# Kernel optimization log

Hardware: AMD Instinct MI355X
Metric: run time of the kernel (lower is better)

The kernel has to match this reference:

```python
import jax, jax.numpy as jnp
import numpy as np

N = 100000
D = 512


def setup_inputs() -> dict:
    key = jax.random.key(0)
    k1, k2 = jax.random.split(key)
    features = jax.random.normal(k1, (N, D), dtype=jnp.float32)
    attn_w = jax.random.normal(k2, (D,), dtype=jnp.float32)
    attn_b = jnp.zeros((1,), dtype=jnp.float32)
    return {"features": features, "attn_w": attn_w, "attn_b": attn_b, "k": 4}


def reference(features, attn_w, attn_b, k):
    # features: [N, D]; sliding-window (half-width k, truncated at edges) mean
    n = features.shape[0]
    zero = jnp.zeros((1, features.shape[1]), dtype=features.dtype)
    cs = jnp.concatenate([zero, jnp.cumsum(features, axis=0)], axis=0)  # [N+1, D]
    i = jnp.arange(n)
    lo = jnp.maximum(i - k, 0)          # inclusive window start
    hi = jnp.minimum(i + k, n - 1)      # inclusive window end
    win_sum = cs[hi + 1] - cs[lo]       # [N, D]
    count = (hi - lo + 1).astype(features.dtype)[:, None]
    agg = win_sum / count               # [N, D] windowed means
    scores = agg @ attn_w + attn_b[0]   # [N]
    w = jax.nn.softmax(scores, axis=0)  # [N]
    bag = w @ agg                       # [D]
    return bag, w
```

## Files before the change

kernel.cpp:

```cpp
#include <hip/hip_runtime.h>
#include <math.h>

#define D 512
#define NB_P 1000

__global__ void k_dot(const float* __restrict__ f, const float* __restrict__ w,
                      float* __restrict__ dot, int n) {
    int wave = threadIdx.x >> 6;
    int lane = threadIdx.x & 63;
    int row  = blockIdx.x * 4 + wave;
    if (row >= n) return;
    const float4* fr = (const float4*)(f + (size_t)row * D);
    const float4* wr = (const float4*)w;
    float4 a0 = fr[lane],      b0 = wr[lane];
    float4 a1 = fr[lane + 64], b1 = wr[lane + 64];
    float s = a0.x*b0.x + a0.y*b0.y + a0.z*b0.z + a0.w*b0.w
            + a1.x*b1.x + a1.y*b1.y + a1.z*b1.z + a1.w*b1.w;
    #pragma unroll
    for (int off = 32; off; off >>= 1) s += __shfl_down(s, off);
    if (lane == 0) dot[row] = s;
}

__global__ void k_scores(const float* __restrict__ dot, const float* __restrict__ bptr,
                         const int* __restrict__ kptr, float* __restrict__ scores,
                         float* __restrict__ pmax, int n) {
    int i = blockIdx.x * blockDim.x + threadIdx.x;
    int k = *kptr;
    float val = -INFINITY;
    if (i < n) {
        int lo = max(i - k, 0), hi = min(i + k, n - 1);
        float s = 0.f;
        for (int j = lo; j <= hi; ++j) s += dot[j];
        val = s / (float)(hi - lo + 1) + bptr[0];
        scores[i] = val;
    }
    float m = val;
    #pragma unroll
    for (int off = 32; off; off >>= 1) m = fmaxf(m, __shfl_down(m, off));
    __shared__ float sm[4];
    int lane = threadIdx.x & 63, wid = threadIdx.x >> 6;
    if (lane == 0) sm[wid] = m;
    __syncthreads();
    if (threadIdx.x == 0) {
        float mm = fmaxf(fmaxf(sm[0], sm[1]), fmaxf(sm[2], sm[3]));
        pmax[blockIdx.x] = mm;
    }
}

__global__ void k_gmax(const float* __restrict__ pmax, int nb, float* __restrict__ scal) {
    float m = -INFINITY;
    for (int i = threadIdx.x; i < nb; i += blockDim.x) m = fmaxf(m, pmax[i]);
    #pragma unroll
    for (int off = 32; off; off >>= 1) m = fmaxf(m, __shfl_down(m, off));
    __shared__ float sm[4];
    int lane = threadIdx.x & 63, wid = threadIdx.x >> 6;
    if (lane == 0) sm[wid] = m;
    __syncthreads();
    if (threadIdx.x == 0) scal[0] = fmaxf(fmaxf(sm[0], sm[1]), fmaxf(sm[2], sm[3]));
}

__global__ void k_exp(float* __restrict__ scores, const float* __restrict__ scal,
                      float* __restrict__ psum, int n) {
    int i = blockIdx.x * blockDim.x + threadIdx.x;
    float gmax = scal[0];
    float e = 0.f;
    if (i < n) {
        e = expf(scores[i] - gmax);
        scores[i] = e;
    }
    #pragma unroll
    for (int off = 32; off; off >>= 1) e += __shfl_down(e, off);
    __shared__ float sm[4];
    int lane = threadIdx.x & 63, wid = threadIdx.x >> 6;
    if (lane == 0) sm[wid] = e;
    __syncthreads();
    if (threadIdx.x == 0) psum[blockIdx.x] = sm[0] + sm[1] + sm[2] + sm[3];
}

__global__ void k_gsum(const float* __restrict__ psum, int nb, float* __restrict__ scal) {
    float s = 0.f;
    for (int i = threadIdx.x; i < nb; i += blockDim.x) s += psum[i];
    #pragma unroll
    for (int off = 32; off; off >>= 1) s += __shfl_down(s, off);
    __shared__ float sm[4];
    int lane = threadIdx.x & 63, wid = threadIdx.x >> 6;
    if (lane == 0) sm[wid] = s;
    __syncthreads();
    if (threadIdx.x == 0) scal[1] = 1.f / (sm[0] + sm[1] + sm[2] + sm[3]);
}

__global__ void k_wu(const float* __restrict__ e, const float* __restrict__ scal,
                     const int* __restrict__ kptr, float* __restrict__ w_out,
                     float* __restrict__ u, int n) {
    int j = blockIdx.x * blockDim.x + threadIdx.x;
    if (j >= n) return;
    int k = *kptr;
    float inv = scal[1];
    w_out[j] = e[j] * inv;
    int lo = max(j - k, 0), hi = min(j + k, n - 1);
    float s = 0.f;
    for (int i = lo; i <= hi; ++i) {
        int li = max(i - k, 0), hh = min(i + k, n - 1);
        s += e[i] / (float)(hh - li + 1);
    }
    u[j] = s * inv;
}

__global__ void k_pbag(const float* __restrict__ f, const float* __restrict__ u,
                       float* __restrict__ partial, int n, int chunk) {
    int t = threadIdx.x;
    int j0 = blockIdx.x * chunk;
    int j1 = min(j0 + chunk, n);
    float4 acc = make_float4(0.f, 0.f, 0.f, 0.f);
    for (int j = j0; j < j1; ++j) {
        float uj = u[j];
        float4 v = ((const float4*)(f + (size_t)j * D))[t];
        acc.x += uj * v.x; acc.y += uj * v.y;
        acc.z += uj * v.z; acc.w += uj * v.w;
    }
    ((float4*)(partial + (size_t)blockIdx.x * D))[t] = acc;
}

__global__ void k_rbag(const float* __restrict__ partial, float* __restrict__ bag, int nb) {
    int c = blockIdx.x * 16 + (threadIdx.x & 15);
    int r = threadIdx.x >> 4;
    float acc = 0.f;
    for (int b = r; b < nb; b += 16) acc += partial[(size_t)b * D + c];
    __shared__ float sm[256];
    sm[threadIdx.x] = acc;
    __syncthreads();
    if (threadIdx.x < 16) {
        float s = 0.f;
        #pragma unroll
        for (int q = 0; q < 16; ++q) s += sm[q * 16 + threadIdx.x];
        bag[blockIdx.x * 16 + threadIdx.x] = s;
    }
}

extern "C" void kernel_launch(void* const* d_in, const int* in_sizes, int n_in,
                              void* d_out, int out_size, void* d_ws, size_t ws_size,
                              hipStream_t stream) {
    const float* f  = (const float*)d_in[0];
    const float* aw = (const float*)d_in[1];
    const float* ab = (const float*)d_in[2];
    const int*   kp = (const int*)d_in[3];
    int n = in_sizes[0] / D;

    float* bag   = (float*)d_out;
    float* w_out = (float*)d_out + D;

    float* wsf    = (float*)d_ws;
    int nb2       = (n + 255) / 256;
    float* dot    = wsf;
    float* scores = wsf + n;
    float* u      = wsf + 2 * (size_t)n;
    float* pmax   = wsf + 3 * (size_t)n;
    float* psum   = pmax + nb2;
    float* scal   = psum + nb2;
    size_t poff   = ((3 * (size_t)n + 2 * (size_t)nb2 + 2) + 15) & ~(size_t)15;
    float* partial = wsf + poff;

    int chunk = (n + NB_P - 1) / NB_P;

    k_dot   <<<(n + 3) / 4, 256, 0, stream>>>(f, aw, dot, n);
    k_scores<<<nb2, 256, 0, stream>>>(dot, ab, kp, scores, pmax, n);
    k_gmax  <<<1, 256, 0, stream>>>(pmax, nb2, scal);
    k_exp   <<<nb2, 256, 0, stream>>>(scores, scal, psum, n);
    k_gsum  <<<1, 256, 0, stream>>>(psum, nb2, scal);
    k_wu    <<<nb2, 256, 0, stream>>>(scores, scal, kp, w_out, u, n);
    k_pbag  <<<NB_P, 128, 0, stream>>>(f, u, partial, n, chunk);
    k_rbag  <<<32, 256, 0, stream>>>(partial, bag, NB_P);
}
```

Baseline: 99.66 us.

## Fuse softmax stages with online max-sum combine and unroll dot/bag kernels

Replaces the separate global-max, exp and sum kernels with an online-softmax scheme. Each score block now records its local max and rescaled exp sum, and one combine kernel merges them. Exponentials are recomputed inside k_wu instead of being stored, which cuts two launches and a pass over the scores. k_dot now handles two rows per wave, k_pbag unrolls by four with independent accumulators, and the number of bag partial blocks doubles. The costs are extra exp work in k_wu, fast-math exp and reciprocal, and a partial buffer twice as large to reduce.

```diff
diff --git a/kernel.cpp b/kernel.cpp
--- a/kernel.cpp
+++ b/kernel.cpp
@@ -2,29 +2,40 @@
 #include <math.h>
 
 #define D 512
-#define NB_P 1000
+#define NB_P 2000
 
 __global__ void k_dot(const float* __restrict__ f, const float* __restrict__ w,
                       float* __restrict__ dot, int n) {
-    int wave = threadIdx.x >> 6;
     int lane = threadIdx.x & 63;
-    int row  = blockIdx.x * 4 + wave;
-    if (row >= n) return;
-    const float4* fr = (const float4*)(f + (size_t)row * D);
+    int wid  = threadIdx.x >> 6;
+    int row0 = (blockIdx.x * 4 + wid) * 2;
+    if (row0 >= n) return;
     const float4* wr = (const float4*)w;
-    float4 a0 = fr[lane],      b0 = wr[lane];
-    float4 a1 = fr[lane + 64], b1 = wr[lane + 64];
-    float s = a0.x*b0.x + a0.y*b0.y + a0.z*b0.z + a0.w*b0.w
-            + a1.x*b1.x + a1.y*b1.y + a1.z*b1.z + a1.w*b1.w;
-    #pragma unroll
-    for (int off = 32; off; off >>= 1) s += __shfl_down(s, off);
-    if (lane == 0) dot[row] = s;
+    float4 b0 = wr[lane], b1 = wr[lane + 64];
+    const float4* fr0 = (const float4*)(f + (size_t)row0 * D);
+    bool has2 = (row0 + 1) < n;
+    const float4* fr1 = (const float4*)(f + (size_t)(has2 ? row0 + 1 : row0) * D);
+    float4 a0 = fr0[lane], a1 = fr0[lane + 64];
+    float4 c0 = fr1[lane], c1 = fr1[lane + 64];
+    float s0 = a0.x*b0.x + a0.y*b0.y + a0.z*b0.z + a0.w*b0.w
+             + a1.x*b1.x + a1.y*b1.y + a1.z*b1.z + a1.w*b1.w;
+    float s1 = c0.x*b0.x + c0.y*b0.y + c0.z*b0.z + c0.w*b0.w
+             + c1.x*b1.x + c1.y*b1.y + c1.z*b1.z + c1.w*b1.w;
+    #pragma unroll
+    for (int off = 32; off; off >>= 1) {
+        s0 += __shfl_down(s0, off);
+        s1 += __shfl_down(s1, off);
+    }
+    if (lane == 0) {
+        dot[row0] = s0;
+        if (has2) dot[row0 + 1] = s1;
+    }
 }
 
 __global__ void k_scores(const float* __restrict__ dot, const float* __restrict__ bptr,
                          const int* __restrict__ kptr, float* __restrict__ scores,
-                         float* __restrict__ pmax, int n) {
-    int i = blockIdx.x * blockDim.x + threadIdx.x;
+                         float* __restrict__ pmax, float* __restrict__ psum, int n) {
+    int i = blockIdx.x * 256 + threadIdx.x;
     int k = *kptr;
     float val = -INFINITY;
     if (i < n) {
@@ -34,74 +45,73 @@
         val = s / (float)(hi - lo + 1) + bptr[0];
         scores[i] = val;
     }
+    __shared__ float sm[4];
+    __shared__ float bmax;
+    int lane = threadIdx.x & 63, wid = threadIdx.x >> 6;
     float m = val;
     #pragma unroll
     for (int off = 32; off; off >>= 1) m = fmaxf(m, __shfl_down(m, off));
+    if (lane == 0) sm[wid] = m;
+    __syncthreads();
+    if (threadIdx.x == 0)
+        bmax = fmaxf(fmaxf(sm[0], sm[1]), fmaxf(sm[2], sm[3]));
+    __syncthreads();
+    float mb = bmax;
+    float e = (i < n) ? __expf(val - mb) : 0.f;
+    #pragma unroll
+    for (int off = 32; off; off >>= 1) e += __shfl_down(e, off);
+    __syncthreads();
+    if (lane == 0) sm[wid] = e;
+    __syncthreads();
+    if (threadIdx.x == 0) {
+        pmax[blockIdx.x] = mb;
+        psum[blockIdx.x] = sm[0] + sm[1] + sm[2] + sm[3];
+    }
+}
+
+__global__ void k_combine(const float* __restrict__ pmax, const float* __restrict__ psum,
+                          int nb, float* __restrict__ scal) {
     __shared__ float sm[4];
+    __shared__ float g;
     int lane = threadIdx.x & 63, wid = threadIdx.x >> 6;
+    float m = -INFINITY;
+    for (int i = threadIdx.x; i < nb; i += 256) m = fmaxf(m, pmax[i]);
+    #pragma unroll
+    for (int off = 32; off; off >>= 1) m = fmaxf(m, __shfl_down(m, off));
     if (lane == 0) sm[wid] = m;
     __syncthreads();
+    if (threadIdx.x == 0)
+        g = fmaxf(fmaxf(sm[0], sm[1]), fmaxf(sm[2], sm[3]));
+    __syncthreads();
+    float gmax = g;
+    float s = 0.f;
+    for (int i = threadIdx.x; i < nb; i += 256) s += psum[i] * __expf(pmax[i] - gmax);
+    #pragma unroll
+    for (int off = 32; off; off >>= 1) s += __shfl_down(s, off);
+    __syncthreads();
+    if (lane == 0) sm[wid] = s;
+    __syncthreads();
     if (threadIdx.x == 0) {
-        float mm = fmaxf(fmaxf(sm[0], sm[1]), fmaxf(sm[2], sm[3]));
-        pmax[blockIdx.x] = mm;
-    }
-}
-
-__global__ void k_gmax(const float* __restrict__ pmax, int nb, float* __restrict__ scal) {
-    float m = -INFINITY;
-    for (int i = threadIdx.x; i < nb; i += blockDim.x) m = fmaxf(m, pmax[i]);
-    #pragma unroll
-    for (int off = 32; off; off >>= 1) m = fmaxf(m, __shfl_down(m, off));
-    __shared__ float sm[4];
-    int lane = threadIdx.x & 63, wid = threadIdx.x >> 6;
-    if (lane == 0) sm[wid] = m;
-    __syncthreads();
-    if (threadIdx.x == 0) scal[0] = fmaxf(fmaxf(sm[0], sm[1]), fmaxf(sm[2], sm[3]));
-}
-
-__global__ void k_exp(float* __restrict__ scores, const float* __restrict__ scal,
-                      float* __restrict__ psum, int n) {
-    int i = blockIdx.x * blockDim.x + threadIdx.x;
-    float gmax = scal[0];
-    float e = 0.f;
-    if (i < n) {
-        e = expf(scores[i] - gmax);
-        scores[i] = e;
-    }
-    #pragma unroll
-    for (int off = 32; off; off >>= 1) e += __shfl_down(e, off);
-    __shared__ float sm[4];
-    int lane = threadIdx.x & 63, wid = threadIdx.x >> 6;
-    if (lane == 0) sm[wid] = e;
-    __syncthreads();
-    if (threadIdx.x == 0) psum[blockIdx.x] = sm[0] + sm[1] + sm[2] + sm[3];
-}
-
-__global__ void k_gsum(const float* __restrict__ psum, int nb, float* __restrict__ scal) {
-    float s = 0.f;
-    for (int i = threadIdx.x; i < nb; i += blockDim.x) s += psum[i];
-    #pragma unroll
-    for (int off = 32; off; off >>= 1) s += __shfl_down(s, off);
-    __shared__ float sm[4];
-    int lane = threadIdx.x & 63, wid = threadIdx.x >> 6;
-    if (lane == 0) sm[wid] = s;
-    __syncthreads();
-    if (threadIdx.x == 0) scal[1] = 1.f / (sm[0] + sm[1] + sm[2] + sm[3]);
-}
-
-__global__ void k_wu(const float* __restrict__ e, const float* __restrict__ scal,
+        scal[0] = gmax;
+        scal[1] = 1.f / (sm[0] + sm[1] + sm[2] + sm[3]);
+    }
+}
+
+__global__ void k_wu(const float* __restrict__ scores, const float* __restrict__ scal,
                      const int* __restrict__ kptr, float* __restrict__ w_out,
                      float* __restrict__ u, int n) {
-    int j = blockIdx.x * blockDim.x + threadIdx.x;
+    int j = blockIdx.x * 256 + threadIdx.x;
     if (j >= n) return;
     int k = *kptr;
-    float inv = scal[1];
-    w_out[j] = e[j] * inv;
+    float gmax = scal[0], inv = scal[1];
+    float ej = __expf(scores[j] - gmax);
+    w_out[j] = ej * inv;
     int lo = max(j - k, 0), hi = min(j + k, n - 1);
     float s = 0.f;
     for (int i = lo; i <= hi; ++i) {
         int li = max(i - k, 0), hh = min(i + k, n - 1);
-        s += e[i] / (float)(hh - li + 1);
+        float e = __expf(scores[i] - gmax);
+        s += e * __builtin_amdgcn_rcpf((float)(hh - li + 1));
     }
     u[j] = s * inv;
 }
@@ -111,14 +121,33 @@
     int t = threadIdx.x;
     int j0 = blockIdx.x * chunk;
     int j1 = min(j0 + chunk, n);
-    float4 acc = make_float4(0.f, 0.f, 0.f, 0.f);
-    for (int j = j0; j < j1; ++j) {
+    float4 acc0 = make_float4(0.f,0.f,0.f,0.f);
+    float4 acc1 = make_float4(0.f,0.f,0.f,0.f);
+    float4 acc2 = make_float4(0.f,0.f,0.f,0.f);
+    float4 acc3 = make_float4(0.f,0.f,0.f,0.f);
+    int j = j0;
+    for (; j + 4 <= j1; j += 4) {
+        float u0 = u[j], u1 = u[j+1], u2 = u[j+2], u3 = u[j+3];
+        float4 v0 = ((const float4*)(f + (size_t)(j  ) * D))[t];
+        float4 v1 = ((const float4*)(f + (size_t)(j+1) * D))[t];
+        float4 v2 = ((const float4*)(f + (size_t)(j+2) * D))[t];
+        float4 v3 = ((const float4*)(f + (size_t)(j+3) * D))[t];
+        acc0.x += u0*v0.x; acc0.y += u0*v0.y; acc0.z += u0*v0.z; acc0.w += u0*v0.w;
+        acc1.x += u1*v1.x; acc1.y += u1*v1.y; acc1.z += u1*v1.z; acc1.w += u1*v1.w;
+        acc2.x += u2*v2.x; acc2.y += u2*v2.y; acc2.z += u2*v2.z; acc2.w += u2*v2.w;
+        acc3.x += u3*v3.x; acc3.y += u3*v3.y; acc3.z += u3*v3.z; acc3.w += u3*v3.w;
+    }
+    for (; j < j1; ++j) {
         float uj = u[j];
         float4 v = ((const float4*)(f + (size_t)j * D))[t];
-        acc.x += uj * v.x; acc.y += uj * v.y;
-        acc.z += uj * v.z; acc.w += uj * v.w;
-    }
-    ((float4*)(partial + (size_t)blockIdx.x * D))[t] = acc;
+        acc0.x += uj*v.x; acc0.y += uj*v.y; acc0.z += uj*v.z; acc0.w += uj*v.w;
+    }
+    float4 a;
+    a.x = (acc0.x + acc1.x) + (acc2.x + acc3.x);
+    a.y = (acc0.y + acc1.y) + (acc2.y + acc3.y);
+    a.z = (acc0.z + acc1.z) + (acc2.z + acc3.z);
+    a.w = (acc0.w + acc1.w) + (acc2.w + acc3.w);
+    ((float4*)(partial + (size_t)blockIdx.x * D))[t] = a;
 }
 
 __global__ void k_rbag(const float* __restrict__ partial, float* __restrict__ bag, int nb) {
@@ -162,12 +191,10 @@
 
     int chunk = (n + NB_P - 1) / NB_P;
 
-    k_dot   <<<(n + 3) / 4, 256, 0, stream>>>(f, aw, dot, n);
-    k_scores<<<nb2, 256, 0, stream>>>(dot, ab, kp, scores, pmax, n);
-    k_gmax  <<<1, 256, 0, stream>>>(pmax, nb2, scal);
-    k_exp   <<<nb2, 256, 0, stream>>>(scores, scal, psum, n);
-    k_gsum  <<<1, 256, 0, stream>>>(psum, nb2, scal);
-    k_wu    <<<nb2, 256, 0, stream>>>(scores, scal, kp, w_out, u, n);
-    k_pbag  <<<NB_P, 128, 0, stream>>>(f, u, partial, n, chunk);
-    k_rbag  <<<32, 256, 0, stream>>>(partial, bag, NB_P);
-}
+    k_dot    <<<(n + 7) / 8, 256, 0, stream>>>(f, aw, dot, n);
+    k_scores <<<nb2, 256, 0, stream>>>(dot, ab, kp, scores, pmax, psum, n);
+    k_combine<<<1, 256, 0, stream>>>(pmax, psum, nb2, scal);
+    k_wu     <<<nb2, 256, 0, stream>>>(scores, scal, kp, w_out, u, n);
+    k_pbag   <<<NB_P, 128, 0, stream>>>(f, u, partial, n, chunk);
+    k_rbag   <<<32, 256, 0, stream>>>(partial, bag, NB_P);
+}
```

Measured after the change: 111.0 us. 11.4% more time.

## Fuse softmax stages via online block max/sum and redundant global reduction

Applied to the files above, without the earlier changes.

Computes each block's local max and its sum of exponentials inside the score kernel, which is the online-softmax rescaling trick. Each block of the weight kernel then redundantly reduces all block partials to get the global max and normalizer, and recomputes exponentials on the fly. This removes three small launches (global max, exp, global sum) and their serialization. The cost is that every block rereads ~391 partials and evaluates more fast-math exponentials, with slightly different numerics.

```diff
diff --git a/kernel.cpp b/kernel.cpp
--- a/kernel.cpp
+++ b/kernel.cpp
@@ -23,8 +23,8 @@
 
 __global__ void k_scores(const float* __restrict__ dot, const float* __restrict__ bptr,
                          const int* __restrict__ kptr, float* __restrict__ scores,
-                         float* __restrict__ pmax, int n) {
-    int i = blockIdx.x * blockDim.x + threadIdx.x;
+                         float* __restrict__ pmax, float* __restrict__ psum, int n) {
+    int i = blockIdx.x * 256 + threadIdx.x;
     int k = *kptr;
     float val = -INFINITY;
     if (i < n) {
@@ -34,76 +34,75 @@
         val = s / (float)(hi - lo + 1) + bptr[0];
         scores[i] = val;
     }
+    __shared__ float sm[4];
+    __shared__ float bmax;
+    int lane = threadIdx.x & 63, wid = threadIdx.x >> 6;
     float m = val;
     #pragma unroll
     for (int off = 32; off; off >>= 1) m = fmaxf(m, __shfl_down(m, off));
-    __shared__ float sm[4];
-    int lane = threadIdx.x & 63, wid = threadIdx.x >> 6;
     if (lane == 0) sm[wid] = m;
     __syncthreads();
+    if (threadIdx.x == 0)
+        bmax = fmaxf(fmaxf(sm[0], sm[1]), fmaxf(sm[2], sm[3]));
+    __syncthreads();
+    float mb = bmax;
+    float e = (i < n) ? __expf(val - mb) : 0.f;
+    #pragma unroll
+    for (int off = 32; off; off >>= 1) e += __shfl_down(e, off);
+    __syncthreads();
+    if (lane == 0) sm[wid] = e;
+    __syncthreads();
     if (threadIdx.x == 0) {
-        float mm = fmaxf(fmaxf(sm[0], sm[1]), fmaxf(sm[2], sm[3]));
-        pmax[blockIdx.x] = mm;
+        pmax[blockIdx.x] = mb;
+        psum[blockIdx.x] = sm[0] + sm[1] + sm[2] + sm[3];
     }
 }
 
-__global__ void k_gmax(const float* __restrict__ pmax, int nb, float* __restrict__ scal) {
+__global__ void k_wu(const float* __restrict__ scores, const float* __restrict__ pmax,
+                     const float* __restrict__ psum, int nb1,
+                     const int* __restrict__ kptr, float* __restrict__ w_out,
+                     float* __restrict__ u, int n) {
+    __shared__ float sm[4];
+    __shared__ float gshared[2];
+    int lane = threadIdx.x & 63, wid = threadIdx.x >> 6;
+
     float m = -INFINITY;
-    for (int i = threadIdx.x; i < nb; i += blockDim.x) m = fmaxf(m, pmax[i]);
+    for (int idx = threadIdx.x; idx < nb1; idx += 256) m = fmaxf(m, pmax[idx]);
     #pragma unroll
     for (int off = 32; off; off >>= 1) m = fmaxf(m, __shfl_down(m, off));
-    __shared__ float sm[4];
-    int lane = threadIdx.x & 63, wid = threadIdx.x >> 6;
     if (lane == 0) sm[wid] = m;
     __syncthreads();
-    if (threadIdx.x == 0) scal[0] = fmaxf(fmaxf(sm[0], sm[1]), fmaxf(sm[2], sm[3]));
-}
+    if (threadIdx.x == 0)
+        gshared[0] = fmaxf(fmaxf(sm[0], sm[1]), fmaxf(sm[2], sm[3]));
+    __syncthreads();
+    float gmax = gshared[0];
 
-__global__ void k_exp(float* __restrict__ scores, const float* __restrict__ scal,
-                      float* __restrict__ psum, int n) {
-    int i = blockIdx.x * blockDim.x + threadIdx.x;
-    float gmax = scal[0];
-    float e = 0.f;
-    if (i < n) {
-        e = expf(scores[i] - gmax);
-        scores[i] = e;
-    }
-    #pragma unroll
-    for (int off = 32; off; off >>= 1) e += __shfl_down(e, off);
-    __shared__ float sm[4];
-    int lane = threadIdx.x & 63, wid = threadIdx.x >> 6;
-    if (lane == 0) sm[wid] = e;
-    __syncthreads();
-    if (threadIdx.x == 0) psum[blockIdx.x] = sm[0] + sm[1] + sm[2] + sm[3];
-}
-
-__global__ void k_gsum(const float* __restrict__ psum, int nb, float* __restrict__ scal) {
     float s = 0.f;
-    for (int i = threadIdx.x; i < nb; i += blockDim.x) s += psum[i];
+    for (int idx = threadIdx.x; idx < nb1; idx += 256)
+        s += psum[idx] * __expf(pmax[idx] - gmax);
     #pragma unroll
     for (int off = 32; off; off >>= 1) s += __shfl_down(s, off);
-    __shared__ float sm[4];
-    int lane = threadIdx.x & 63, wid = threadIdx.x >> 6;
+    __syncthreads();
     if (lane == 0) sm[wid] = s;
     __syncthreads();
-    if (threadIdx.x == 0) scal[1] = 1.f / (sm[0] + sm[1] + sm[2] + sm[3]);
-}
+    if (threadIdx.x == 0)
+        gshared[1] = 1.f / (sm[0] + sm[1] + sm[2] + sm[3]);
+    __syncthreads();
+    float inv = gshared[1];
 
-__global__ void k_wu(const float* __restrict__ e, const float* __restrict__ scal,
-                     const int* __restrict__ kptr, float* __restrict__ w_out,
-                     float* __restrict__ u, int n) {
-    int j = blockIdx.x * blockDim.x + threadIdx.x;
+    int j = blockIdx.x * 256 + threadIdx.x;
     if (j >= n) return;
     int k = *kptr;
-    float inv = scal[1];
-    w_out[j] = e[j] * inv;
+    float ej = __expf(scores[j] - gmax);
+    w_out[j] = ej * inv;
     int lo = max(j - k, 0), hi = min(j + k, n - 1);
-    float s = 0.f;
+    float acc = 0.f;
     for (int i = lo; i <= hi; ++i) {
         int li = max(i - k, 0), hh = min(i + k, n - 1);
-        s += e[i] / (float)(hh - li + 1);
+        float e = __expf(scores[i] - gmax);
+        acc += e * __builtin_amdgcn_rcpf((float)(hh - li + 1));
     }
-    u[j] = s * inv;
+    u[j] = acc * inv;
 }
 
 __global__ void k_pbag(const float* __restrict__ f, const float* __restrict__ u,
@@ -149,25 +148,22 @@
     float* bag   = (float*)d_out;
     float* w_out = (float*)d_out + D;
 
-    float* wsf    = (float*)d_ws;
-    int nb2       = (n + 255) / 256;
-    float* dot    = wsf;
-    float* scores = wsf + n;
-    float* u      = wsf + 2 * (size_t)n;
-    float* pmax   = wsf + 3 * (size_t)n;
-    float* psum   = pmax + nb2;
-    float* scal   = psum + nb2;
-    size_t poff   = ((3 * (size_t)n + 2 * (size_t)nb2 + 2) + 15) & ~(size_t)15;
+    int nb2 = (n + 255) / 256;
+
+    float* wsf     = (float*)d_ws;
+    float* dot     = wsf;
+    float* scores  = wsf + n;
+    float* u       = wsf + 2 * (size_t)n;
+    float* pmax    = wsf + 3 * (size_t)n;
+    float* psum    = pmax + nb2;
+    size_t poff    = ((3 * (size_t)n + 2 * (size_t)nb2) + 31) & ~(size_t)31;
     float* partial = wsf + poff;
 
     int chunk = (n + NB_P - 1) / NB_P;
 
     k_dot   <<<(n + 3) / 4, 256, 0, stream>>>(f, aw, dot, n);
-    k_scores<<<nb2, 256, 0, stream>>>(dot, ab, kp, scores, pmax, n);
-    k_gmax  <<<1, 256, 0, stream>>>(pmax, nb2, scal);
-    k_exp   <<<nb2, 256, 0, stream>>>(scores, scal, psum, n);
-    k_gsum  <<<1, 256, 0, stream>>>(psum, nb2, scal);
-    k_wu    <<<nb2, 256, 0, stream>>>(scores, scal, kp, w_out, u, n);
+    k_scores<<<nb2, 256, 0, stream>>>(dot, ab, kp, scores, pmax, psum, n);
+    k_wu    <<<nb2, 256, 0, stream>>>(scores, pmax, psum, nb2, kp, w_out, u, n);
     k_pbag  <<<NB_P, 128, 0, stream>>>(f, u, partial, n, chunk);
     k_rbag  <<<32, 256, 0, stream>>>(partial, bag, NB_P);
 }
```

New measurement: 96.15 us. 1.04x faster.
